# Kernel tuning notes

Hardware: AMD Instinct MI355X
Metric: run time of the kernel (lower is better)

The kernel has to match this reference:

```python
import jax, jax.numpy as jnp
import numpy as np

# ---- static configuration (mirrors repo globals) ----
D_MODEL = 1024   # d_model
B = 128          # batch size
T = 256          # structure sequence length (tgt)
T_C = 128        # max constraints per scene (tgt_c rows)
N_PER = 64       # real (non-padded) constraints per scene
S = 128          # number of source objects per scene (src_e rows)
N_TYPES = 4      # len(constraint_types)
N_DIR = 4        # len(direction_types)
C_TOKEN = 2      # structure_vocab_map['c']
N_C = N_PER * B  # total constraints across the batch (static!)


def setup_inputs() -> dict:
    key = jax.random.key(0)
    ks = jax.random.split(key, 12)
    decoded_output = jax.random.normal(ks[0], (T, B, D_MODEL), jnp.float32)
    # tgt: the first N_PER timesteps of every batch element are constraint tokens 'c'.
    tgt = jnp.where(jnp.arange(T)[:, None] < N_PER, C_TOKEN, 0) * jnp.ones((1, B), jnp.int32)
    tgt = tgt.astype(jnp.int32)
    # tgt_c padding: rows >= N_PER are padding -> exactly N_PER*B = N_C real constraints,
    # laid out row-major (timestep-major, batch-fastest) when flattened.
    tgt_c_padding_mask = jnp.broadcast_to(jnp.arange(T_C)[:, None] >= N_PER, (T_C, B))
    types_col = jax.random.randint(ks[1], (T_C, B), 0, N_TYPES)
    q_col = jax.random.randint(ks[2], (T_C, B), 0, S)
    r_col = jax.random.randint(ks[3], (T_C, B), 0, S)
    tgt_c = jnp.stack([types_col, q_col, r_col], axis=-1).astype(jnp.int32)  # [T_C,B,3]
    src_e = jax.random.normal(ks[4], (S, B, D_MODEL), jnp.float32)
    src_padding_mask = jax.random.uniform(ks[5], (B, S)) < 0.1
    scale = 0.02
    params = {
        'type_emb': jax.random.normal(ks[6], (N_TYPES, D_MODEL), jnp.float32),
        'W_ctype': jax.random.normal(ks[7], (N_TYPES, D_MODEL), jnp.float32) * scale,
        'b_ctype': jnp.zeros((N_TYPES,), jnp.float32),
        'W_obj': jax.random.normal(ks[8], (D_MODEL, 3 * D_MODEL), jnp.float32) * scale,
        'b_obj': jnp.zeros((D_MODEL,), jnp.float32),
        'W_dir': jax.random.normal(ks[9], (N_DIR, 4 * D_MODEL), jnp.float32) * scale,
        'b_dir': jnp.zeros((N_DIR,), jnp.float32),
    }
    return dict(decoded_output=decoded_output, tgt=tgt, tgt_c=tgt_c,
                tgt_c_padding_mask=tgt_c_padding_mask, src_e=src_e,
                src_padding_mask=src_padding_mask, **params)


def reference(decoded_output, tgt, tgt_c, tgt_c_padding_mask, src_e, src_padding_mask,
              type_emb, W_ctype, b_ctype, W_obj, b_obj, W_dir, b_dir):
    d = decoded_output.shape[-1]
    # --- static-count boolean selections (setup guarantees exactly N_C True entries) ---
    idx_struct = jnp.nonzero((tgt == C_TOKEN).reshape(-1), size=N_C)[0]
    heads = decoded_output.reshape(-1, d)[idx_struct]                # [N_C, d]
    idx_c = jnp.nonzero((~tgt_c_padding_mask).reshape(-1), size=N_C)[0]

    # constraint type logits
    type_selections = heads @ W_ctype.T + b_ctype                    # [N_C, N_TYPES]

    # constraint type embeddings
    types = type_emb[tgt_c[:, :, 0].reshape(-1)[idx_c]]              # [N_C, d]

    # q_e: gather query-object embeddings (torch.gather along dim 0)
    q_idx = jnp.broadcast_to(tgt_c[:, :, 1:2], (T_C, B, d))
    q_e = jnp.take_along_axis(src_e, q_idx, axis=0).reshape(-1, d)[idx_c]  # [N_C, d]

    obj_in = jnp.concatenate([heads, types, q_e], axis=1)            # [N_C, 3d]
    pointer = obj_in @ W_obj.T + b_obj                               # [N_C, d]

    batch_ref = jnp.broadcast_to(jnp.arange(B), (T_C, B)).reshape(-1)[idx_c]  # [N_C]
    # Setup layout guarantee: flattened constraint order is (t, b) row-major with b
    # fastest, N_PER constraints per batch -> pointer reshapes to [N_PER, B, d] and the
    # original per-item tensordot loop collapses into one batched einsum.
    ptr = pointer.reshape(N_PER, B, d)
    logits = jnp.einsum('tbd,sbd->tbs', ptr, src_e).reshape(N_C, S)  # [N_C, S]
    object_selections = jnp.where(src_padding_mask[batch_ref], -jnp.inf, logits)

    # r_e: gather reference-object embeddings
    r_idx = jnp.broadcast_to(tgt_c[:, :, 2:3], (T_C, B, d))
    r_e = jnp.take_along_axis(src_e, r_idx, axis=0).reshape(-1, d)[idx_c]    # [N_C, d]

    dir_in = jnp.concatenate([obj_in, r_e], axis=1)                  # [N_C, 4d]
    direction_selections = dir_in @ W_dir.T + b_dir                  # [N_C, N_DIR]
    return (type_selections, object_selections, direction_selections)
```

## Files before the change

### kernel.cpp

```cpp
#include <hip/hip_runtime.h>
#include <hip/hip_bf16.h>
#include <math.h>

#define D_MODEL 1024
#define B_SZ    128
#define S_SZ    128
#define N_C     8192
#define K_OBJ   3072
#define K_DIR   4096

#define TS_OFF  0
#define OS_OFF  (N_C * 4)
#define DS_OFF  (OS_OFF + N_C * S_SZ)

#define NEG_BIG (-1.0e30f)

typedef __attribute__((ext_vector_type(8))) int   i32x8;
typedef __attribute__((ext_vector_type(4))) float f32x4;

#define WS_PTR8   0ull
#define WS_DEC8   8388608ull
#define WS_SRCE8  16777216ull
#define WS_WOBJ8  33554432ull
#define WS_TEMB8  36700160ull

#define SCALE_ONE 0x7F7F7F7F

__device__ __forceinline__ uint2 f32x8_to_fp8(float4 a, float4 b) {
    unsigned lo = 0, hi = 0;
    lo = __builtin_amdgcn_cvt_pk_fp8_f32(a.x, a.y, lo, false);
    lo = __builtin_amdgcn_cvt_pk_fp8_f32(a.z, a.w, lo, true);
    hi = __builtin_amdgcn_cvt_pk_fp8_f32(b.x, b.y, hi, false);
    hi = __builtin_amdgcn_cvt_pk_fp8_f32(b.z, b.w, hi, true);
    return make_uint2(lo, hi);
}
__device__ __forceinline__ unsigned char f32_to_fp8(float x) {
    return (unsigned char)(__builtin_amdgcn_cvt_pk_fp8_f32(x, x, 0, false) & 0xFF);
}

typedef __attribute__((address_space(3))) unsigned int lds_u32;
typedef __attribute__((address_space(1))) const unsigned int glb_u32;
__device__ __forceinline__ void dma16(const void* g, void* l) {
    __builtin_amdgcn_global_load_lds((glb_u32*)g, (lds_u32*)l, 16, 0, 0);
}

__global__ __launch_bounds__(256) void cvt_fp8_all(
    const float* __restrict__ src_e,   const float* __restrict__ W_obj,
    const float* __restrict__ type_emb,
    unsigned char* __restrict__ srce8, unsigned char* __restrict__ wobj8,
    unsigned char* __restrict__ temb8)
{
    const int blk = blockIdx.x;
    const float* src; unsigned char* dst; size_t u;
    if (blk < 8192)       { src = src_e;    dst = srce8; u = (size_t)blk * 256 + threadIdx.x; }
    else if (blk < 9728)  { src = W_obj;    dst = wobj8; u = (size_t)(blk - 8192) * 256 + threadIdx.x; }
    else                  { src = type_emb; dst = temb8; u = (size_t)(blk - 9728) * 256 + threadIdx.x; }
    const float4* s = (const float4*)src + u * 2;
    float4 a = s[0], b = s[1];
    *(uint2*)(dst + u * 8) = f32x8_to_fp8(a, b);
}

__global__ __launch_bounds__(256) void pointer_fp8(
    const unsigned char* __restrict__ dec8,
    const unsigned char* __restrict__ temb8,
    const unsigned char* __restrict__ srce8,
    const unsigned char* __restrict__ wobj8,
    const int*   __restrict__ tgt_c,
    const float* __restrict__ b_obj,
    unsigned char* __restrict__ ptr_out)
{
    __shared__ __align__(32) unsigned char As[2][128 * 128];
    __shared__ __align__(32) unsigned char Bs[2][128 * 128];

    const int tid  = threadIdx.x;
    const int m0   = blockIdx.x * 128;
    const int n0   = blockIdx.y * 128;
    const int lane = tid & 63;
    const int wv   = tid >> 6;

    const int srow = wv * 8 + (lane >> 3);
    const int c16  = lane & 7;
    const unsigned char *pA0[4], *pA1[4], *pA2[4], *pB[4];
    #pragma unroll
    for (int ro = 0; ro < 4; ++ro) {
        int r = ro * 32 + srow;
        int g = (c16 ^ ((r & 3) << 1)) * 16;
        int n = m0 + r;
        int tt = tgt_c[n * 3 + 0];
        int qq = tgt_c[n * 3 + 1];
        pA0[ro] = dec8  + (size_t)n * 1024 + g;
        pA1[ro] = temb8 + (size_t)tt * 1024 + g;
        pA2[ro] = srce8 + ((size_t)qq * B_SZ + r) * 1024 + g;
        pB[ro]  = wobj8 + (size_t)(n0 + r) * K_OBJ + g;
    }

    const int wm   = (wv & 1) * 64;
    const int wn   = (wv >> 1) * 64;
    const int fm   = lane & 15;
    const int quad = lane >> 4;

    f32x4 acc[4][4];
    #pragma unroll
    for (int i = 0; i < 4; ++i)
        #pragma unroll
        for (int j = 0; j < 4; ++j)
            acc[i][j] = (f32x4){0.f, 0.f, 0.f, 0.f};

    #pragma unroll
    for (int ro = 0; ro < 4; ++ro) {
        dma16(pA0[ro], &As[0][ro * 4096 + wv * 1024]);
        dma16(pB[ro],  &Bs[0][ro * 4096 + wv * 1024]);
    }
    __syncthreads();

    for (int ks = 0; ks < K_OBJ / 128; ++ks) {
        const int buf = ks & 1;

        if (ks + 1 < K_OBJ / 128) {
            const int k0n   = (ks + 1) * 128;
            const int regn  = k0n >> 10;
            const int koffn = k0n & 1023;
            #pragma unroll
            for (int ro = 0; ro < 4; ++ro) {
                void* la = &As[buf ^ 1][ro * 4096 + wv * 1024];
                if (regn == 0)      dma16(pA0[ro] + koffn, la);
                else if (regn == 1) dma16(pA1[ro] + koffn, la);
                else                dma16(pA2[ro] + koffn, la);
                dma16(pB[ro] + k0n, &Bs[buf ^ 1][ro * 4096 + wv * 1024]);
            }
        }

        i32x8 af[4], bfr[4];
        #pragma unroll
        for (int i = 0; i < 4; ++i) {
            int ra = wm + i * 16 + fm;
            af[i] = *(const i32x8*)&As[buf][ra * 128 + ((quad ^ (ra & 3)) << 5)];
        }
        #pragma unroll
        for (int j = 0; j < 4; ++j) {
            int rb = wn + j * 16 + fm;
            bfr[j] = *(const i32x8*)&Bs[buf][rb * 128 + ((quad ^ (rb & 3)) << 5)];
        }
        #pragma unroll
        for (int i = 0; i < 4; ++i)
            #pragma unroll
            for (int j = 0; j < 4; ++j)
                acc[i][j] = __builtin_amdgcn_mfma_scale_f32_16x16x128_f8f6f4(
                    af[i], bfr[j], acc[i][j], 0, 0, 0, SCALE_ONE, 0, SCALE_ONE);

        __syncthreads();
    }

    #pragma unroll
    for (int j = 0; j < 4; ++j) {
        int ncol = n0 + wn + j * 16 + fm;
        float bo = b_obj[ncol];
        #pragma unroll
        for (int i = 0; i < 4; ++i) {
            int mrow = m0 + wm + i * 16 + quad * 4;
            f32x4 c = acc[i][j];
            #pragma unroll
            for (int r2 = 0; r2 < 4; ++r2)
                ptr_out[(size_t)(mrow + r2) * D_MODEL + ncol] = f32_to_fp8(c[r2] + bo);
        }
    }
}

__global__ __launch_bounds__(256) void logits_fp8(
    const unsigned char* __restrict__ ptr8,
    const unsigned char* __restrict__ srce8,
    const void*  __restrict__ src_pm,
    float*       __restrict__ out_os)
{
    __shared__ __align__(32) unsigned char As[2][64 * 128];
    __shared__ __align__(32) unsigned char Bs[2][64 * 128];
    __shared__ int s_flag;

    const int tid  = threadIdx.x;
    const int b    = blockIdx.x;
    const int s0   = blockIdx.y * 64;
    const int lane = tid & 63;
    const int wv   = tid >> 6;

    if (tid == 0) s_flag = 0;
    __syncthreads();
    {
        const int* pmi = (const int*)src_pm;
        int local = 0;
        for (int i = tid; i < 4096; i += 256) local |= (pmi[i] > 1);
        if (local) atomicOr(&s_flag, 1);
    }

    const int srow = wv * 8 + (lane >> 3);
    const int c16  = lane & 7;
    const unsigned char *pA[2], *pBt[2];
    #pragma unroll
    for (int ro = 0; ro < 2; ++ro) {
        int r = ro * 32 + srow;
        int g = (c16 ^ ((r & 3) << 1)) * 16;
        pA[ro]  = ptr8  + ((size_t)r * B_SZ + b) * 1024 + g;
        pBt[ro] = srce8 + ((size_t)(s0 + r) * B_SZ + b) * 1024 + g;
    }

    const int wm   = (wv & 1) * 32;
    const int wn   = (wv >> 1) * 32;
    const int fm   = lane & 15;
    const int quad = lane >> 4;

    f32x4 acc[2][2];
    #pragma unroll
    for (int i = 0; i < 2; ++i)
        #pragma unroll
        for (int j = 0; j < 2; ++j)
            acc[i][j] = (f32x4){0.f, 0.f, 0.f, 0.f};

    #pragma unroll
    for (int ro = 0; ro < 2; ++ro) {
        dma16(pA[ro],  &As[0][ro * 4096 + wv * 1024]);
        dma16(pBt[ro], &Bs[0][ro * 4096 + wv * 1024]);
    }
    __syncthreads();

    for (int ks = 0; ks < D_MODEL / 128; ++ks) {
        const int buf = ks & 1;

        if (ks + 1 < D_MODEL / 128) {
            const int k0n = (ks + 1) * 128;
            #pragma unroll
            for (int ro = 0; ro < 2; ++ro) {
                dma16(pA[ro]  + k0n, &As[buf ^ 1][ro * 4096 + wv * 1024]);
                dma16(pBt[ro] + k0n, &Bs[buf ^ 1][ro * 4096 + wv * 1024]);
            }
        }

        i32x8 af[2], bfr[2];
        #pragma unroll
        for (int i = 0; i < 2; ++i) {
            int ra = wm + i * 16 + fm;
            af[i] = *(const i32x8*)&As[buf][ra * 128 + ((quad ^ (ra & 3)) << 5)];
        }
        #pragma unroll
        for (int j = 0; j < 2; ++j) {
            int rb = wn + j * 16 + fm;
            bfr[j] = *(const i32x8*)&Bs[buf][rb * 128 + ((quad ^ (rb & 3)) << 5)];
        }
        #pragma unroll
        for (int i = 0; i < 2; ++i)
            #pragma unroll
            for (int j = 0; j < 2; ++j)
                acc[i][j] = __builtin_amdgcn_mfma_scale_f32_16x16x128_f8f6f4(
                    af[i], bfr[j], acc[i][j], 0, 0, 0, SCALE_ONE, 0, SCALE_ONE);

        __syncthreads();
    }

    const bool u8 = (s_flag != 0);
    const unsigned char* pm8  = (const unsigned char*)src_pm;
    const int*           pm32 = (const int*)src_pm;

    #pragma unroll
    for (int j = 0; j < 2; ++j) {
        int s = s0 + wn + j * 16 + fm;
        bool m = u8 ? (pm8[b * S_SZ + s] != 0) : (pm32[b * S_SZ + s] != 0);
        #pragma unroll
        for (int i = 0; i < 2; ++i) {
            int t = wm + i * 16 + quad * 4;
            f32x4 c = acc[i][j];
            #pragma unroll
            for (int r2 = 0; r2 < 4; ++r2)
                out_os[(size_t)((t + r2) * B_SZ + b) * S_SZ + s] = m ? NEG_BIG : c[r2];
        }
    }
}

__global__ __launch_bounds__(256) void typedir_kernel(
    const float* __restrict__ decoded,
    const int*   __restrict__ tgt_c,
    const float* __restrict__ src_e,
    const float* __restrict__ type_emb,
    const float* __restrict__ W_ctype,
    const float* __restrict__ b_ctype,
    const float* __restrict__ W_dir,
    const float* __restrict__ b_dir,
    unsigned char* __restrict__ dec8,
    float*       __restrict__ out)
{
    const int tid = threadIdx.x;
    const int n0  = blockIdx.x * 4;
    const int kc  = tid * 4;

    __shared__ int s_idx[4][3];
    if (tid < 12) s_idx[tid / 3][tid % 3] = tgt_c[(n0 + tid / 3) * 3 + (tid % 3)];
    __syncthreads();

    float acct[4][4] = {};
    float accd[4][4] = {};

    #pragma unroll
    for (int it = 0; it < 4; ++it) {
        float4 wd[4];
        #pragma unroll
        for (int c = 0; c < 4; ++c)
            wd[c] = *(const float4*)&W_dir[(size_t)c * K_DIR + it * 1024 + kc];
        float4 wc[4];
        if (it == 0) {
            #pragma unroll
            for (int c = 0; c < 4; ++c)
                wc[c] = *(const float4*)&W_ctype[(size_t)c * D_MODEL + kc];
        }

        #pragma unroll
        for (int r = 0; r < 4; ++r) {
            const int n = n0 + r;
            const int b = n & 127;
            float4 a;
            if (it == 0) {
                a = *(const float4*)&decoded[(size_t)n * D_MODEL + kc];
                unsigned pk = __builtin_amdgcn_cvt_pk_fp8_f32(a.x, a.y, 0u, false);
                pk = __builtin_amdgcn_cvt_pk_fp8_f32(a.z, a.w, pk, true);
                *(unsigned*)(dec8 + (size_t)n * D_MODEL + kc) = pk;
            } else if (it == 1) {
                a = *(const float4*)&type_emb[(size_t)s_idx[r][0] * D_MODEL + kc];
            } else if (it == 2) {
                a = *(const float4*)&src_e[((size_t)s_idx[r][1] * B_SZ + b) * D_MODEL + kc];
            } else {
                a = *(const float4*)&src_e[((size_t)s_idx[r][2] * B_SZ + b) * D_MODEL + kc];
            }

            #pragma unroll
            for (int c = 0; c < 4; ++c)
                accd[r][c] += a.x * wd[c].x + a.y * wd[c].y
                            + a.z * wd[c].z + a.w * wd[c].w;
            if (it == 0) {
                #pragma unroll
                for (int c = 0; c < 4; ++c)
                    acct[r][c] += a.x * wc[c].x + a.y * wc[c].y
                                + a.z * wc[c].z + a.w * wc[c].w;
            }
        }
    }

    __shared__ float red[4][32];
    const int lane = tid & 63;
    const int wave = tid >> 6;

    float vals[32];
    #pragma unroll
    for (int r = 0; r < 4; ++r)
        #pragma unroll
        for (int c = 0; c < 4; ++c) {
            vals[r * 4 + c]      = acct[r][c];
            vals[16 + r * 4 + c] = accd[r][c];
        }

    #pragma unroll
    for (int x = 0; x < 32; ++x) {
        float v = vals[x];
        #pragma unroll
        for (int off = 32; off > 0; off >>= 1)
            v += __shfl_down(v, off, 64);
        vals[x] = v;
    }
    if (lane == 0)
        #pragma unroll
        for (int x = 0; x < 32; ++x) red[wave][x] = vals[x];
    __syncthreads();

    if (tid < 32) {
        float v = red[0][tid] + red[1][tid] + red[2][tid] + red[3][tid];
        int r = (tid & 15) >> 2;
        int c = tid & 3;
        int n = n0 + r;
        if (tid < 16) out[TS_OFF + (size_t)n * 4 + c] = v + b_ctype[c];
        else          out[DS_OFF + (size_t)n * 4 + c] = v + b_dir[c];
    }
}

extern "C" void kernel_launch(void* const* d_in, const int* in_sizes, int n_in,
                              void* d_out, int out_size, void* d_ws, size_t ws_size,
                              hipStream_t stream) {
    const float* decoded  = (const float*)d_in[0];
    const int*   tgt_c    = (const int*)d_in[2];
    const float* src_e    = (const float*)d_in[4];
    const void*  src_pm   = d_in[5];
    const float* type_emb = (const float*)d_in[6];
    const float* W_ctype  = (const float*)d_in[7];
    const float* b_ctype  = (const float*)d_in[8];
    const float* W_obj    = (const float*)d_in[9];
    const float* b_obj    = (const float*)d_in[10];
    const float* W_dir    = (const float*)d_in[11];
    const float* b_dir    = (const float*)d_in[12];

    float* out = (float*)d_out;
    char*  ws  = (char*)d_ws;
    unsigned char* ptr8  = (unsigned char*)(ws + WS_PTR8);
    unsigned char* dec8  = (unsigned char*)(ws + WS_DEC8);
    unsigned char* srce8 = (unsigned char*)(ws + WS_SRCE8);
    unsigned char* wobj8 = (unsigned char*)(ws + WS_WOBJ8);
    unsigned char* temb8 = (unsigned char*)(ws + WS_TEMB8);

    cvt_fp8_all<<<9730, 256, 0, stream>>>(
        src_e, W_obj, type_emb, srce8, wobj8, temb8);

    typedir_kernel<<<N_C / 4, 256, 0, stream>>>(
        decoded, tgt_c, src_e, type_emb, W_ctype, b_ctype, W_dir, b_dir,
        dec8, out);

    pointer_fp8<<<dim3(N_C / 128, D_MODEL / 128), 256, 0, stream>>>(
        dec8, temb8, srce8, wobj8, tgt_c, b_obj, ptr8);

    logits_fp8<<<dim3(B_SZ, 2), 256, 0, stream>>>(
        ptr8, srce8, src_pm, out + OS_OFF);
}
```

Before: 290.2 us.

## Merge fp8 conversion into prep kernel and deepen pointer GEMM A-tile pipeline

The separate fp8 conversion kernel is folded into the type/direction kernel as extra blocks, saving one launch and letting conversion overlap with the typedir work. The pointer GEMM moves to a triple-buffered A tile and double-buffered B tile. It prefetches A two stages ahead and waits with explicit vmcnt counts plus a raw barrier instead of a full __syncthreads at the end of each iteration. This is meant to hide the latency of gathered A loads, at the cost of more LDS per block (80KB), which may reduce occupancy.

Result: no change. 286.1 us, median of 2 (-1.4%).

```diff
diff --git a/kernel.cpp b/kernel.cpp
--- a/kernel.cpp
+++ b/kernel.cpp
@@ -44,236 +44,7 @@
     __builtin_amdgcn_global_load_lds((glb_u32*)g, (lds_u32*)l, 16, 0, 0);
 }
 
-__global__ __launch_bounds__(256) void cvt_fp8_all(
-    const float* __restrict__ src_e,   const float* __restrict__ W_obj,
-    const float* __restrict__ type_emb,
-    unsigned char* __restrict__ srce8, unsigned char* __restrict__ wobj8,
-    unsigned char* __restrict__ temb8)
-{
-    const int blk = blockIdx.x;
-    const float* src; unsigned char* dst; size_t u;
-    if (blk < 8192)       { src = src_e;    dst = srce8; u = (size_t)blk * 256 + threadIdx.x; }
-    else if (blk < 9728)  { src = W_obj;    dst = wobj8; u = (size_t)(blk - 8192) * 256 + threadIdx.x; }
-    else                  { src = type_emb; dst = temb8; u = (size_t)(blk - 9728) * 256 + threadIdx.x; }
-    const float4* s = (const float4*)src + u * 2;
-    float4 a = s[0], b = s[1];
-    *(uint2*)(dst + u * 8) = f32x8_to_fp8(a, b);
-}
-
-__global__ __launch_bounds__(256) void pointer_fp8(
-    const unsigned char* __restrict__ dec8,
-    const unsigned char* __restrict__ temb8,
-    const unsigned char* __restrict__ srce8,
-    const unsigned char* __restrict__ wobj8,
-    const int*   __restrict__ tgt_c,
-    const float* __restrict__ b_obj,
-    unsigned char* __restrict__ ptr_out)
-{
-    __shared__ __align__(32) unsigned char As[2][128 * 128];
-    __shared__ __align__(32) unsigned char Bs[2][128 * 128];
-
-    const int tid  = threadIdx.x;
-    const int m0   = blockIdx.x * 128;
-    const int n0   = blockIdx.y * 128;
-    const int lane = tid & 63;
-    const int wv   = tid >> 6;
-
-    const int srow = wv * 8 + (lane >> 3);
-    const int c16  = lane & 7;
-    const unsigned char *pA0[4], *pA1[4], *pA2[4], *pB[4];
-    #pragma unroll
-    for (int ro = 0; ro < 4; ++ro) {
-        int r = ro * 32 + srow;
-        int g = (c16 ^ ((r & 3) << 1)) * 16;
-        int n = m0 + r;
-        int tt = tgt_c[n * 3 + 0];
-        int qq = tgt_c[n * 3 + 1];
-        pA0[ro] = dec8  + (size_t)n * 1024 + g;
-        pA1[ro] = temb8 + (size_t)tt * 1024 + g;
-        pA2[ro] = srce8 + ((size_t)qq * B_SZ + r) * 1024 + g;
-        pB[ro]  = wobj8 + (size_t)(n0 + r) * K_OBJ + g;
-    }
-
-    const int wm   = (wv & 1) * 64;
-    const int wn   = (wv >> 1) * 64;
-    const int fm   = lane & 15;
-    const int quad = lane >> 4;
-
-    f32x4 acc[4][4];
-    #pragma unroll
-    for (int i = 0; i < 4; ++i)
-        #pragma unroll
-        for (int j = 0; j < 4; ++j)
-            acc[i][j] = (f32x4){0.f, 0.f, 0.f, 0.f};
-
-    #pragma unroll
-    for (int ro = 0; ro < 4; ++ro) {
-        dma16(pA0[ro], &As[0][ro * 4096 + wv * 1024]);
-        dma16(pB[ro],  &Bs[0][ro * 4096 + wv * 1024]);
-    }
-    __syncthreads();
-
-    for (int ks = 0; ks < K_OBJ / 128; ++ks) {
-        const int buf = ks & 1;
-
-        if (ks + 1 < K_OBJ / 128) {
-            const int k0n   = (ks + 1) * 128;
-            const int regn  = k0n >> 10;
-            const int koffn = k0n & 1023;
-            #pragma unroll
-            for (int ro = 0; ro < 4; ++ro) {
-                void* la = &As[buf ^ 1][ro * 4096 + wv * 1024];
-                if (regn == 0)      dma16(pA0[ro] + koffn, la);
-                else if (regn == 1) dma16(pA1[ro] + koffn, la);
-                else                dma16(pA2[ro] + koffn, la);
-                dma16(pB[ro] + k0n, &Bs[buf ^ 1][ro * 4096 + wv * 1024]);
-            }
-        }
-
-        i32x8 af[4], bfr[4];
-        #pragma unroll
-        for (int i = 0; i < 4; ++i) {
-            int ra = wm + i * 16 + fm;
-            af[i] = *(const i32x8*)&As[buf][ra * 128 + ((quad ^ (ra & 3)) << 5)];
-        }
-        #pragma unroll
-        for (int j = 0; j < 4; ++j) {
-            int rb = wn + j * 16 + fm;
-            bfr[j] = *(const i32x8*)&Bs[buf][rb * 128 + ((quad ^ (rb & 3)) << 5)];
-        }
-        #pragma unroll
-        for (int i = 0; i < 4; ++i)
-            #pragma unroll
-            for (int j = 0; j < 4; ++j)
-                acc[i][j] = __builtin_amdgcn_mfma_scale_f32_16x16x128_f8f6f4(
-                    af[i], bfr[j], acc[i][j], 0, 0, 0, SCALE_ONE, 0, SCALE_ONE);
-
-        __syncthreads();
-    }
-
-    #pragma unroll
-    for (int j = 0; j < 4; ++j) {
-        int ncol = n0 + wn + j * 16 + fm;
-        float bo = b_obj[ncol];
-        #pragma unroll
-        for (int i = 0; i < 4; ++i) {
-            int mrow = m0 + wm + i * 16 + quad * 4;
-            f32x4 c = acc[i][j];
-            #pragma unroll
-            for (int r2 = 0; r2 < 4; ++r2)
-                ptr_out[(size_t)(mrow + r2) * D_MODEL + ncol] = f32_to_fp8(c[r2] + bo);
-        }
-    }
-}
-
-__global__ __launch_bounds__(256) void logits_fp8(
-    const unsigned char* __restrict__ ptr8,
-    const unsigned char* __restrict__ srce8,
-    const void*  __restrict__ src_pm,
-    float*       __restrict__ out_os)
-{
-    __shared__ __align__(32) unsigned char As[2][64 * 128];
-    __shared__ __align__(32) unsigned char Bs[2][64 * 128];
-    __shared__ int s_flag;
-
-    const int tid  = threadIdx.x;
-    const int b    = blockIdx.x;
-    const int s0   = blockIdx.y * 64;
-    const int lane = tid & 63;
-    const int wv   = tid >> 6;
-
-    if (tid == 0) s_flag = 0;
-    __syncthreads();
-    {
-        const int* pmi = (const int*)src_pm;
-        int local = 0;
-        for (int i = tid; i < 4096; i += 256) local |= (pmi[i] > 1);
-        if (local) atomicOr(&s_flag, 1);
-    }
-
-    const int srow = wv * 8 + (lane >> 3);
-    const int c16  = lane & 7;
-    const unsigned char *pA[2], *pBt[2];
-    #pragma unroll
-    for (int ro = 0; ro < 2; ++ro) {
-        int r = ro * 32 + srow;
-        int g = (c16 ^ ((r & 3) << 1)) * 16;
-        pA[ro]  = ptr8  + ((size_t)r * B_SZ + b) * 1024 + g;
-        pBt[ro] = srce8 + ((size_t)(s0 + r) * B_SZ + b) * 1024 + g;
-    }
-
-    const int wm   = (wv & 1) * 32;
-    const int wn   = (wv >> 1) * 32;
-    const int fm   = lane & 15;
-    const int quad = lane >> 4;
-
-    f32x4 acc[2][2];
-    #pragma unroll
-    for (int i = 0; i < 2; ++i)
-        #pragma unroll
-        for (int j = 0; j < 2; ++j)
-            acc[i][j] = (f32x4){0.f, 0.f, 0.f, 0.f};
-
-    #pragma unroll
-    for (int ro = 0; ro < 2; ++ro) {
-        dma16(pA[ro],  &As[0][ro * 4096 + wv * 1024]);
-        dma16(pBt[ro], &Bs[0][ro * 4096 + wv * 1024]);
-    }
-    __syncthreads();
-
-    for (int ks = 0; ks < D_MODEL / 128; ++ks) {
-        const int buf = ks & 1;
-
-        if (ks + 1 < D_MODEL / 128) {
-            const int k0n = (ks + 1) * 128;
-            #pragma unroll
-            for (int ro = 0; ro < 2; ++ro) {
-                dma16(pA[ro]  + k0n, &As[buf ^ 1][ro * 4096 + wv * 1024]);
-                dma16(pBt[ro] + k0n, &Bs[buf ^ 1][ro * 4096 + wv * 1024]);
-            }
-        }
-
-        i32x8 af[2], bfr[2];
-        #pragma unroll
-        for (int i = 0; i < 2; ++i) {
-            int ra = wm + i * 16 + fm;
-            af[i] = *(const i32x8*)&As[buf][ra * 128 + ((quad ^ (ra & 3)) << 5)];
-        }
-        #pragma unroll
-        for (int j = 0; j < 2; ++j) {
-            int rb = wn + j * 16 + fm;
-            bfr[j] = *(const i32x8*)&Bs[buf][rb * 128 + ((quad ^ (rb & 3)) << 5)];
-        }
-        #pragma unroll
-        for (int i = 0; i < 2; ++i)
-            #pragma unroll
-            for (int j = 0; j < 2; ++j)
-                acc[i][j] = __builtin_amdgcn_mfma_scale_f32_16x16x128_f8f6f4(
-                    af[i], bfr[j], acc[i][j], 0, 0, 0, SCALE_ONE, 0, SCALE_ONE);
-
-        __syncthreads();
-    }
-
-    const bool u8 = (s_flag != 0);
-    const unsigned char* pm8  = (const unsigned char*)src_pm;
-    const int*           pm32 = (const int*)src_pm;
-
-    #pragma unroll
-    for (int j = 0; j < 2; ++j) {
-        int s = s0 + wn + j * 16 + fm;
-        bool m = u8 ? (pm8[b * S_SZ + s] != 0) : (pm32[b * S_SZ + s] != 0);
-        #pragma unroll
-        for (int i = 0; i < 2; ++i) {
-            int t = wm + i * 16 + quad * 4;
-            f32x4 c = acc[i][j];
-            #pragma unroll
-            for (int r2 = 0; r2 < 4; ++r2)
-                out_os[(size_t)((t + r2) * B_SZ + b) * S_SZ + s] = m ? NEG_BIG : c[r2];
-        }
-    }
-}
-
-__global__ __launch_bounds__(256) void typedir_kernel(
+__global__ __launch_bounds__(256) void prep_kernel(
     const float* __restrict__ decoded,
     const int*   __restrict__ tgt_c,
     const float* __restrict__ src_e,
@@ -282,12 +53,29 @@
     const float* __restrict__ b_ctype,
     const float* __restrict__ W_dir,
     const float* __restrict__ b_dir,
+    const float* __restrict__ W_obj,
     unsigned char* __restrict__ dec8,
+    unsigned char* __restrict__ srce8,
+    unsigned char* __restrict__ wobj8,
+    unsigned char* __restrict__ temb8,
     float*       __restrict__ out)
 {
     const int tid = threadIdx.x;
-    const int n0  = blockIdx.x * 4;
-    const int kc  = tid * 4;
+
+    if (blockIdx.x >= 2048) {
+        const int cblk = blockIdx.x - 2048;
+        const float* src; unsigned char* dst; size_t u;
+        if (cblk < 8192)      { src = src_e;    dst = srce8; u = (size_t)cblk * 256 + tid; }
+        else if (cblk < 9728) { src = W_obj;    dst = wobj8; u = (size_t)(cblk - 8192) * 256 + tid; }
+        else                  { src = type_emb; dst = temb8; u = (size_t)(cblk - 9728) * 256 + tid; }
+        const float4* s = (const float4*)src + u * 2;
+        float4 a = s[0], b = s[1];
+        *(uint2*)(dst + u * 8) = f32x8_to_fp8(a, b);
+        return;
+    }
+
+    const int n0 = blockIdx.x * 4;
+    const int kc = tid * 4;
 
     __shared__ int s_idx[4][3];
     if (tid < 12) s_idx[tid / 3][tid % 3] = tgt_c[(n0 + tid / 3) * 3 + (tid % 3)];
@@ -376,6 +164,230 @@
     }
 }
 
+__global__ __launch_bounds__(256) void pointer_fp8(
+    const unsigned char* __restrict__ dec8,
+    const unsigned char* __restrict__ temb8,
+    const unsigned char* __restrict__ srce8,
+    const unsigned char* __restrict__ wobj8,
+    const int*   __restrict__ tgt_c,
+    const float* __restrict__ b_obj,
+    unsigned char* __restrict__ ptr_out)
+{
+    __shared__ __align__(32) unsigned char As[3][128 * 128];
+    __shared__ __align__(32) unsigned char Bs[2][128 * 128];
+
+    const int tid  = threadIdx.x;
+    const int m0   = blockIdx.x * 128;
+    const int n0   = blockIdx.y * 128;
+    const int lane = tid & 63;
+    const int wv   = tid >> 6;
+    const int NK   = K_OBJ / 128;
+
+    const int srow = wv * 8 + (lane >> 3);
+    const int c16  = lane & 7;
+    const unsigned char *pA0[4], *pA1[4], *pA2[4], *pB[4];
+    #pragma unroll
+    for (int ro = 0; ro < 4; ++ro) {
+        int r = ro * 32 + srow;
+        int g = (c16 ^ ((r & 3) << 1)) * 16;
+        int n = m0 + r;
+        int tt = tgt_c[n * 3 + 0];
+        int qq = tgt_c[n * 3 + 1];
+        pA0[ro] = dec8  + (size_t)n * 1024 + g;
+        pA1[ro] = temb8 + (size_t)tt * 1024 + g;
+        pA2[ro] = srce8 + ((size_t)qq * B_SZ + r) * 1024 + g;
+        pB[ro]  = wobj8 + (size_t)(n0 + r) * K_OBJ + g;
+    }
+
+    auto stageA = [&](int t, int abuf) {
+        const int k0   = t * 128;
+        const int reg  = k0 >> 10;
+        const int koff = k0 & 1023;
+        #pragma unroll
+        for (int ro = 0; ro < 4; ++ro) {
+            void* la = &As[abuf][ro * 4096 + wv * 1024];
+            if (reg == 0)      dma16(pA0[ro] + koff, la);
+            else if (reg == 1) dma16(pA1[ro] + koff, la);
+            else               dma16(pA2[ro] + koff, la);
+        }
+    };
+    auto stageB = [&](int t) {
+        const int k0 = t * 128;
+        #pragma unroll
+        for (int ro = 0; ro < 4; ++ro)
+            dma16(pB[ro] + k0, &Bs[t & 1][ro * 4096 + wv * 1024]);
+    };
+
+    const int wm   = (wv & 1) * 64;
+    const int wn   = (wv >> 1) * 64;
+    const int fm   = lane & 15;
+    const int quad = lane >> 4;
+
+    f32x4 acc[4][4];
+    #pragma unroll
+    for (int i = 0; i < 4; ++i)
+        #pragma unroll
+        for (int j = 0; j < 4; ++j)
+            acc[i][j] = (f32x4){0.f, 0.f, 0.f, 0.f};
+
+    stageB(0);
+    stageA(0, 0);
+    stageA(1, 1);
+
+    int a_cur = 0;
+    for (int ks = 0; ks < NK; ++ks) {
+        if (ks < NK - 1) asm volatile("s_waitcnt vmcnt(4)" ::: "memory");
+        else             asm volatile("s_waitcnt vmcnt(0)" ::: "memory");
+        __builtin_amdgcn_s_barrier();
+        asm volatile("" ::: "memory");
+
+        const int a_stage = (a_cur == 0) ? 2 : a_cur - 1;
+        if (ks + 1 < NK) stageB(ks + 1);
+        if (ks + 2 < NK) stageA(ks + 2, a_stage);
+
+        i32x8 af[4], bfr[4];
+        #pragma unroll
+        for (int i = 0; i < 4; ++i) {
+            int ra = wm + i * 16 + fm;
+            af[i] = *(const i32x8*)&As[a_cur][ra * 128 + ((quad ^ (ra & 3)) << 5)];
+        }
+        #pragma unroll
+        for (int j = 0; j < 4; ++j) {
+            int rb = wn + j * 16 + fm;
+            bfr[j] = *(const i32x8*)&Bs[ks & 1][rb * 128 + ((quad ^ (rb & 3)) << 5)];
+        }
+        #pragma unroll
+        for (int i = 0; i < 4; ++i)
+            #pragma unroll
+            for (int j = 0; j < 4; ++j)
+                acc[i][j] = __builtin_amdgcn_mfma_scale_f32_16x16x128_f8f6f4(
+                    af[i], bfr[j], acc[i][j], 0, 0, 0, SCALE_ONE, 0, SCALE_ONE);
+
+        a_cur = (a_cur == 2) ? 0 : a_cur + 1;
+    }
+
+    #pragma unroll
+    for (int j = 0; j < 4; ++j) {
+        int ncol = n0 + wn + j * 16 + fm;
+        float bo = b_obj[ncol];
+        #pragma unroll
+        for (int i = 0; i < 4; ++i) {
+            int mrow = m0 + wm + i * 16 + quad * 4;
+            f32x4 c = acc[i][j];
+            #pragma unroll
+            for (int r2 = 0; r2 < 4; ++r2)
+                ptr_out[(size_t)(mrow + r2) * D_MODEL + ncol] = f32_to_fp8(c[r2] + bo);
+        }
+    }
+}
+
+__global__ __launch_bounds__(256) void logits_fp8(
+    const unsigned char* __restrict__ ptr8,
+    const unsigned char* __restrict__ srce8,
+    const void*  __restrict__ src_pm,
+    float*       __restrict__ out_os)
+{
+    __shared__ __align__(32) unsigned char As[2][64 * 128];
+    __shared__ __align__(32) unsigned char Bs[2][64 * 128];
+    __shared__ int s_flag;
+
+    const int tid  = threadIdx.x;
+    const int b    = blockIdx.x;
+    const int s0   = blockIdx.y * 64;
+    const int lane = tid & 63;
+    const int wv   = tid >> 6;
+
+    if (tid == 0) s_flag = 0;
+    __syncthreads();
+    {
+        const int* pmi = (const int*)src_pm;
+        int local = 0;
+        for (int i = tid; i < 4096; i += 256) local |= (pmi[i] > 1);
+        if (local) atomicOr(&s_flag, 1);
+    }
+
+    const int srow = wv * 8 + (lane >> 3);
+    const int c16  = lane & 7;
+    const unsigned char *pA[2], *pBt[2];
+    #pragma unroll
+    for (int ro = 0; ro < 2; ++ro) {
+        int r = ro * 32 + srow;
+        int g = (c16 ^ ((r & 3) << 1)) * 16;
+        pA[ro]  = ptr8  + ((size_t)r * B_SZ + b) * 1024 + g;
+        pBt[ro] = srce8 + ((size_t)(s0 + r) * B_SZ + b) * 1024 + g;
+    }
+
+    const int wm   = (wv & 1) * 32;
+    const int wn   = (wv >> 1) * 32;
+    const int fm   = lane & 15;
+    const int quad = lane >> 4;
+
+    f32x4 acc[2][2];
+    #pragma unroll
+    for (int i = 0; i < 2; ++i)
+        #pragma unroll
+        for (int j = 0; j < 2; ++j)
+            acc[i][j] = (f32x4){0.f, 0.f, 0.f, 0.f};
+
+    #pragma unroll
+    for (int ro = 0; ro < 2; ++ro) {
+        dma16(pA[ro],  &As[0][ro * 4096 + wv * 1024]);
+        dma16(pBt[ro], &Bs[0][ro * 4096 + wv * 1024]);
+    }
+    __syncthreads();
+
+    for (int ks = 0; ks < D_MODEL / 128; ++ks) {
+        const int buf = ks & 1;
+
+        if (ks + 1 < D_MODEL / 128) {
+            const int k0n = (ks + 1) * 128;
+            #pragma unroll
+            for (int ro = 0; ro < 2; ++ro) {
+                dma16(pA[ro]  + k0n, &As[buf ^ 1][ro * 4096 + wv * 1024]);
+                dma16(pBt[ro] + k0n, &Bs[buf ^ 1][ro * 4096 + wv * 1024]);
+            }
+        }
+
+        i32x8 af[2], bfr[2];
+        #pragma unroll
+        for (int i = 0; i < 2; ++i) {
+            int ra = wm + i * 16 + fm;
+            af[i] = *(const i32x8*)&As[buf][ra * 128 + ((quad ^ (ra & 3)) << 5)];
+        }
+        #pragma unroll
+        for (int j = 0; j < 2; ++j) {
+            int rb = wn + j * 16 + fm;
+            bfr[j] = *(const i32x8*)&Bs[buf][rb * 128 + ((quad ^ (rb & 3)) << 5)];
+        }
+        #pragma unroll
+        for (int i = 0; i < 2; ++i)
+            #pragma unroll
+            for (int j = 0; j < 2; ++j)
+                acc[i][j] = __builtin_amdgcn_mfma_scale_f32_16x16x128_f8f6f4(
+                    af[i], bfr[j], acc[i][j], 0, 0, 0, SCALE_ONE, 0, SCALE_ONE);
+
+        __syncthreads();
+    }
+
+    const bool u8 = (s_flag != 0);
+    const unsigned char* pm8  = (const unsigned char*)src_pm;
+    const int*           pm32 = (const int*)src_pm;
+
+    #pragma unroll
+    for (int j = 0; j < 2; ++j) {
+        int s = s0 + wn + j * 16 + fm;
+        bool m = u8 ? (pm8[b * S_SZ + s] != 0) : (pm32[b * S_SZ + s] != 0);
+        #pragma unroll
+        for (int i = 0; i < 2; ++i) {
+            int t = wm + i * 16 + quad * 4;
+            f32x4 c = acc[i][j];
+            #pragma unroll
+            for (int r2 = 0; r2 < 4; ++r2)
+                out_os[(size_t)((t + r2) * B_SZ + b) * S_SZ + s] = m ? NEG_BIG : c[r2];
+        }
+    }
+}
+
 extern "C" void kernel_launch(void* const* d_in, const int* in_sizes, int n_in,
                               void* d_out, int out_size, void* d_ws, size_t ws_size,
                               hipStream_t stream) {
@@ -399,12 +411,9 @@
     unsigned char* wobj8 = (unsigned char*)(ws + WS_WOBJ8);
     unsigned char* temb8 = (unsigned char*)(ws + WS_TEMB8);
 
-    cvt_fp8_all<<<9730, 256, 0, stream>>>(
-        src_e, W_obj, type_emb, srce8, wobj8, temb8);
-
-    typedir_kernel<<<N_C / 4, 256, 0, stream>>>(
+    prep_kernel<<<11778, 256, 0, stream>>>(
         decoded, tgt_c, src_e, type_emb, W_ctype, b_ctype, W_dir, b_dir,
-        dec8, out);
+        W_obj, dec8, srce8, wobj8, temb8, out);
 
     pointer_fp8<<<dim3(N_C / 128, D_MODEL / 128), 256, 0, stream>>>(
         dec8, temb8, srce8, wobj8, tgt_c, b_obj, ptr8);
```
